# Kernel optimization log

Measured on AMD Instinct MI355X. Metric: run time of the kernel, lower is better.

## Reference

```python
import jax, jax.numpy as jnp
import numpy as np

EMBED_DIM = 1024
NUM_HEADS = 16
HEAD_DIM = EMBED_DIM // NUM_HEADS
BATCH = 2
SEQ = 2048


def setup_inputs() -> dict:
    key = jax.random.key(0)
    ks = jax.random.split(key, 9)
    s = 1.0 / np.sqrt(EMBED_DIM)
    return {
        "x": jax.random.normal(ks[0], (BATCH, SEQ, EMBED_DIM), jnp.float32),
        "mask": jnp.ones((BATCH, SEQ), jnp.int32),
        "Wq": jax.random.normal(ks[1], (EMBED_DIM, EMBED_DIM), jnp.float32) * s,
        "bq": jax.random.normal(ks[2], (EMBED_DIM,), jnp.float32) * s,
        "Wk": jax.random.normal(ks[3], (EMBED_DIM, EMBED_DIM), jnp.float32) * s,
        "bk": jax.random.normal(ks[4], (EMBED_DIM,), jnp.float32) * s,
        "Wv": jax.random.normal(ks[5], (EMBED_DIM, EMBED_DIM), jnp.float32) * s,
        "bv": jax.random.normal(ks[6], (EMBED_DIM,), jnp.float32) * s,
        "Wo": jax.random.normal(ks[7], (EMBED_DIM, EMBED_DIM), jnp.float32) * s,
        "bo": jax.random.normal(ks[8], (EMBED_DIM,), jnp.float32) * s,
    }


def reference(x, mask, Wq, bq, Wk, bk, Wv, bv, Wo, bo):
    B, S, E = x.shape
    H, D = NUM_HEADS, HEAD_DIM
    # torch Linear: y = x @ W.T + b
    q = (x @ Wq.T + bq).reshape(B, S, H, D).transpose(0, 2, 1, 3)  # [B,H,S,D]
    k = (x @ Wk.T + bk).reshape(B, S, H, D).transpose(0, 2, 1, 3)
    v = (x @ Wv.T + bv).reshape(B, S, H, D).transpose(0, 2, 1, 3)
    scores = jnp.einsum("bhqd,bhkd->bhqk", q, k) / jnp.sqrt(jnp.float32(D))
    # mask: [B,S] -> [B,1,1,S]; fill masked positions with -1e9
    scores = jnp.where(mask[:, None, None, :] == 0, jnp.float32(-1e9), scores)
    probs = jax.nn.softmax(scores, axis=-1)
    # dropout omitted: original stores a float and would crash; eval semantics = identity
    attn = jnp.einsum("bhqk,bhkd->bhqd", probs, v)  # [B,H,S,D]
    attn = attn.transpose(0, 2, 1, 3).reshape(B, S, E)
    return attn @ Wo.T + bo
```

## Files before the change

### kernel.cpp

```cpp
#include <hip/hip_runtime.h>
#include <stdint.h>

#define S_LEN 2048
#define EMB   1024
#define NH    16
#define HD    64
#define BM 128
#define BN 128
#define BK 64

typedef __bf16 bf16x8 __attribute__((ext_vector_type(8)));
typedef short  short4v __attribute__((ext_vector_type(4)));
typedef unsigned int uint2v __attribute__((ext_vector_type(2)));
typedef float  floatx4 __attribute__((ext_vector_type(4)));

#if defined(__has_builtin)
#if __has_builtin(__builtin_amdgcn_mfma_f32_16x16x16bf16_1k)
#define HAVE_MFMA16 1
#endif
#if __has_builtin(__builtin_amdgcn_exp2f)
#define EXP2F(x) __builtin_amdgcn_exp2f(x)
#endif
#endif
#ifndef EXP2F
#define EXP2F(x) exp2f(x)
#endif

#define QSCALE 0.1803368801111204f

__device__ __forceinline__ unsigned short f2bf(float f) {
  unsigned u = __builtin_bit_cast(unsigned, f);
  u += 0x7fffu + ((u >> 16) & 1u);
  return (unsigned short)(u >> 16);
}

__global__ __launch_bounds__(256) void cvt_all(const float* __restrict__ x,
                                               const float* __restrict__ Wq,
                                               const float* __restrict__ Wk,
                                               const float* __restrict__ Wv,
                                               const float* __restrict__ Wo,
                                               unsigned short* __restrict__ xb,
                                               unsigned short* __restrict__ Wqb,
                                               unsigned short* __restrict__ Wkb,
                                               unsigned short* __restrict__ Wvb,
                                               unsigned short* __restrict__ Wob) {
  int blk = blockIdx.x;
  const float* s; unsigned short* d; int off;
  if (blk < 4096)      { s = x;  d = xb;  off = blk; }
  else if (blk < 5120) { s = Wq; d = Wqb; off = blk - 4096; }
  else if (blk < 6144) { s = Wk; d = Wkb; off = blk - 5120; }
  else if (blk < 7168) { s = Wv; d = Wvb; off = blk - 6144; }
  else                 { s = Wo; d = Wob; off = blk - 7168; }
  int i = (off * 256 + threadIdx.x) * 4;
  float4 v = *(const float4*)(s + i);
  ushort4 o;
  o.x = f2bf(v.x); o.y = f2bf(v.y); o.z = f2bf(v.z); o.w = f2bf(v.w);
  *(ushort4*)(d + i) = o;
}

__device__ __forceinline__ void stage16(const void* g, void* l) {
  __builtin_amdgcn_global_load_lds(
      (const __attribute__((address_space(1))) void*)g,
      (__attribute__((address_space(3))) void*)l, 16, 0, 0);
}

__device__ __forceinline__ void gemm128(const unsigned short* __restrict__ A,
                                        const unsigned short* __restrict__ Bm,
                                        const float* __restrict__ bias, float scale,
                                        void* __restrict__ outp, int mode,
                                        unsigned short* As, unsigned short* Bs) {
  const int tid  = threadIdx.x;
  const int lane = tid & 63;
  const int wave = tid >> 6;
  const int m16  = lane & 15;
  const int quad = lane >> 4;
  const int m0 = blockIdx.x * BM;
  const int n0 = blockIdx.y * BN;
  const int wrow = (wave >> 1) * 64;
  const int wcol = (wave & 1) * 64;
  const int K = 1024, N = 1024;

  floatx4 acc[4][4];
  for (int i = 0; i < 4; ++i)
    for (int j = 0; j < 4; ++j) acc[i][j] = floatx4{0.f, 0.f, 0.f, 0.f};

  for (int k0 = 0; k0 < K; k0 += BK) {
    __syncthreads();
    for (int i = 0; i < 4; ++i) {
      int c   = i * 256 + tid;
      int row = c >> 3;
      int col = (c & 7) << 3;
      stage16(A  + (size_t)(m0 + row) * K + k0 + col,
              (char*)As + (size_t)(i * 256 + wave * 64) * 16);
      stage16(Bm + (size_t)(n0 + row) * K + k0 + col,
              (char*)Bs + (size_t)(i * 256 + wave * 64) * 16);
    }
    __syncthreads();
    for (int kk = 0; kk < 2; ++kk) {
      bf16x8 af[4], bfr[4];
      for (int ti = 0; ti < 4; ++ti)
        af[ti] = *(const bf16x8*)(As + (wrow + ti * 16 + m16) * BK + kk * 32 + quad * 8);
      for (int tj = 0; tj < 4; ++tj)
        bfr[tj] = *(const bf16x8*)(Bs + (wcol + tj * 16 + m16) * BK + kk * 32 + quad * 8);
      if (mode == 2) {
        for (int ti = 0; ti < 4; ++ti)
          for (int tj = 0; tj < 4; ++tj)
            acc[ti][tj] = __builtin_amdgcn_mfma_f32_16x16x32_bf16(bfr[tj], af[ti], acc[ti][tj], 0, 0, 0);
      } else {
        for (int ti = 0; ti < 4; ++ti)
          for (int tj = 0; tj < 4; ++tj)
            acc[ti][tj] = __builtin_amdgcn_mfma_f32_16x16x32_bf16(af[ti], bfr[tj], acc[ti][tj], 0, 0, 0);
      }
    }
  }

  if (mode == 2) {
    for (int tj = 0; tj < 4; ++tj) {
      for (int reg = 0; reg < 4; ++reg) {
        int n = n0 + wcol + tj * 16 + quad * 4 + reg;
        int hh = n >> 6, d = n & 63;
        float bv = bias[n];
        for (int ti = 0; ti < 4; ++ti) {
          int m = m0 + wrow + ti * 16 + m16;
          int b = m >> 11, s = m & 2047;
          ((unsigned short*)outp)[((size_t)(b * NH + hh) * HD + d) * S_LEN + s] =
              f2bf(acc[ti][tj][reg] + bv);
        }
      }
    }
    return;
  }

  for (int tj = 0; tj < 4; ++tj) {
    int n = n0 + wcol + tj * 16 + m16;
    float bv = bias[n];
    for (int ti = 0; ti < 4; ++ti) {
      for (int reg = 0; reg < 4; ++reg) {
        int m = m0 + wrow + ti * 16 + quad * 4 + reg;
        float v = (acc[ti][tj][reg] + bv) * scale;
        if (mode == 0) {
          ((float*)outp)[(size_t)m * N + n] = v;
        } else {
          int b = m >> 11, s = m & 2047, hh = n >> 6, d = n & 63;
          ((unsigned short*)outp)[((size_t)(b * NH + hh) * S_LEN + s) * HD + d] = f2bf(v);
        }
      }
    }
  }
}

__global__ __launch_bounds__(256) void qkv_gemm(const unsigned short* __restrict__ xb,
                                                const unsigned short* __restrict__ Wqb,
                                                const unsigned short* __restrict__ Wkb,
                                                const unsigned short* __restrict__ Wvb,
                                                const float* __restrict__ bq,
                                                const float* __restrict__ bk,
                                                const float* __restrict__ bv,
                                                unsigned short* __restrict__ Qb,
                                                unsigned short* __restrict__ Kb,
                                                unsigned short* __restrict__ Vtb) {
  __shared__ unsigned short As[BM * BK];
  __shared__ unsigned short Bs[BN * BK];
  int z = blockIdx.z;
  const unsigned short* Bm = (z == 0) ? Wqb : (z == 1) ? Wkb : Wvb;
  const float* bias        = (z == 0) ? bq  : (z == 1) ? bk  : bv;
  unsigned short* outp     = (z == 0) ? Qb  : (z == 1) ? Kb  : Vtb;
  float scale = (z == 0) ? QSCALE : 1.0f;
  gemm128(xb, Bm, bias, scale, outp, (z == 2) ? 2 : 1, As, Bs);
}

__global__ __launch_bounds__(256) void out_gemm(const unsigned short* __restrict__ Ab,
                                                const unsigned short* __restrict__ Wob,
                                                const float* __restrict__ bo,
                                                float* __restrict__ out) {
  __shared__ unsigned short As[64 * BK];
  __shared__ unsigned short Bs[128 * BK];
  const int tid  = threadIdx.x;
  const int lane = tid & 63;
  const int wave = tid >> 6;
  const int m16  = lane & 15;
  const int quad = lane >> 4;
  const int m0 = blockIdx.x * 64;
  const int n0 = blockIdx.y * 128;
  const int wrow = (wave >> 1) * 32;
  const int wcol = (wave & 1) * 64;
  const int K = 1024, N = 1024;

  floatx4 acc[2][4];
  for (int i = 0; i < 2; ++i)
    for (int j = 0; j < 4; ++j) acc[i][j] = floatx4{0.f, 0.f, 0.f, 0.f};

  for (int k0 = 0; k0 < K; k0 += BK) {
    __syncthreads();
    for (int i = 0; i < 2; ++i) {
      int c = i * 256 + tid;
      int row = c >> 3, col = (c & 7) << 3;
      stage16(Ab + (size_t)(m0 + row) * K + k0 + col,
              (char*)As + (size_t)(i * 256 + wave * 64) * 16);
    }
    for (int i = 0; i < 4; ++i) {
      int c = i * 256 + tid;
      int row = c >> 3, col = (c & 7) << 3;
      stage16(Wob + (size_t)(n0 + row) * K + k0 + col,
              (char*)Bs + (size_t)(i * 256 + wave * 64) * 16);
    }
    __syncthreads();
    for (int kk = 0; kk < 2; ++kk) {
      bf16x8 af[2], bfr[4];
      for (int ti = 0; ti < 2; ++ti)
        af[ti] = *(const bf16x8*)(As + (wrow + ti * 16 + m16) * BK + kk * 32 + quad * 8);
      for (int tj = 0; tj < 4; ++tj)
        bfr[tj] = *(const bf16x8*)(Bs + (wcol + tj * 16 + m16) * BK + kk * 32 + quad * 8);
      for (int ti = 0; ti < 2; ++ti)
        for (int tj = 0; tj < 4; ++tj)
          acc[ti][tj] = __builtin_amdgcn_mfma_f32_16x16x32_bf16(af[ti], bfr[tj], acc[ti][tj], 0, 0, 0);
    }
  }

  for (int tj = 0; tj < 4; ++tj) {
    int n = n0 + wcol + tj * 16 + m16;
    float bv = bo[n];
    for (int ti = 0; ti < 2; ++ti)
      for (int reg = 0; reg < 4; ++reg) {
        int m = m0 + wrow + ti * 16 + quad * 4 + reg;
        out[(size_t)m * N + n] = acc[ti][tj][reg] + bv;
      }
  }
}

__global__ __launch_bounds__(512, 2) void attn_kernel(const unsigned short* __restrict__ Qb,
                                                      const unsigned short* __restrict__ Kb,
                                                      const unsigned short* __restrict__ Vtb,
                                                      const int* __restrict__ mask,
                                                      unsigned short* __restrict__ attnb) {
  __shared__ unsigned short Ks[128 * 64];
  __shared__ unsigned short Vts[64 * 128];
  __shared__ float mb[128];
#ifndef HAVE_MFMA16
  __shared__ unsigned short Pq[8 * 16 * 72];
#endif

  const int tid  = threadIdx.x;
  const int lane = tid & 63;
  const int wave = tid >> 6;
  const int m16  = lane & 15;
  const int quad = lane >> 4;
  const int bh = blockIdx.x;
  const int qt = blockIdx.y;
  const int b  = bh >> 4;
  const int h  = bh & 15;
  const int q0 = qt * 128;
  const size_t head = (size_t)bh * S_LEN * HD;

  bf16x8 qf[2];
  {
    const unsigned short* qrow = Qb + head + (size_t)(q0 + wave * 16 + m16) * HD;
    qf[0] = *(const bf16x8*)(qrow + quad * 8);
    qf[1] = *(const bf16x8*)(qrow + 32 + quad * 8);
  }

  const int krow = tid >> 3, kch = tid & 7;
  const unsigned short* kg = Kb + head + (size_t)krow * HD + kch * 8;
  unsigned short* kl = Ks + krow * 64 + (kch ^ (krow & 7)) * 8;
  const int vrow = tid >> 4, vch = tid & 15;
  const unsigned short* vg = Vtb + head + (size_t)vrow * S_LEN + vch * 8;
  unsigned short* vl = Vts + vrow * 128 + (vch ^ (vrow & 7)) * 8;

  float m_run = -1e30f, l_run = 0.f;
  floatx4 acc_o[4];
  for (int ti = 0; ti < 4; ++ti) acc_o[ti] = floatx4{0.f, 0.f, 0.f, 0.f};

  uint4 kp0 = *(const uint4*)(kg);
  uint4 kp1 = *(const uint4*)(kg + 64 * HD);
  uint4 vp0 = *(const uint4*)(vg);
  uint4 vp1 = *(const uint4*)(vg + 32 * S_LEN);
  int   mp  = (tid < 128) ? mask[b * S_LEN + tid] : 1;

  const int xs = m16 & 7;

  for (int kb = 0; kb < 16; ++kb) {
    __syncthreads();
    *(uint4*)kl = kp0;  *(uint4*)(kl + 64 * 64) = kp1;
    *(uint4*)vl = vp0;  *(uint4*)(vl + 32 * 128) = vp1;
    if (tid < 128) mb[tid] = (mp == 0) ? -1e9f : 0.f;
    __syncthreads();

    {
      int kvn = (kb + 1 < 16) ? (kb + 1) * 128 : 0;
      kp0 = *(const uint4*)(kg + (size_t)kvn * HD);
      kp1 = *(const uint4*)(kg + (size_t)(kvn + 64) * HD);
      vp0 = *(const uint4*)(vg + kvn);
      vp1 = *(const uint4*)(vg + 32 * S_LEN + kvn);
      if (tid < 128) mp = mask[b * S_LEN + kvn + tid];
    }

    for (int hf = 0; hf < 2; ++hf) {
      floatx4 acc_s[4];
      for (int tj = 0; tj < 4; ++tj) acc_s[tj] = floatx4{0.f, 0.f, 0.f, 0.f};
      for (int kk = 0; kk < 2; ++kk)
        for (int tj = 0; tj < 4; ++tj) {
          bf16x8 kf = *(const bf16x8*)&Ks[(hf * 64 + tj * 16 + m16) * 64 +
                                          (((kk * 4 + quad) ^ xs) << 3)];
          acc_s[tj] = __builtin_amdgcn_mfma_f32_16x16x32_bf16(kf, qf[kk], acc_s[tj], 0, 0, 0);
        }

      float s[16];
      for (int t = 0; t < 4; ++t) {
        float4 mv = *(const float4*)&mb[hf * 64 + t * 16 + quad * 4];
        s[t * 4 + 0] = acc_s[t][0] + mv.x;
        s[t * 4 + 1] = acc_s[t][1] + mv.y;
        s[t * 4 + 2] = acc_s[t][2] + mv.z;
        s[t * 4 + 3] = acc_s[t][3] + mv.w;
      }
      float mloc = fmaxf(fmaxf(fmaxf(s[0], s[1]), fmaxf(s[2], s[3])),
                         fmaxf(fmaxf(s[4], s[5]), fmaxf(s[6], s[7])));
      float mloc2 = fmaxf(fmaxf(fmaxf(s[8], s[9]), fmaxf(s[10], s[11])),
                          fmaxf(fmaxf(s[12], s[13]), fmaxf(s[14], s[15])));
      mloc = fmaxf(mloc, mloc2);
      mloc = fmaxf(mloc, __shfl_xor(mloc, 16));
      mloc = fmaxf(mloc, __shfl_xor(mloc, 32));

      if (__any(mloc > m_run)) {
        float mnew = fmaxf(m_run, mloc);
        float alpha = EXP2F(m_run - mnew);
        m_run = mnew;
        l_run *= alpha;
        for (int ti = 0; ti < 4; ++ti)
          for (int reg = 0; reg < 4; ++reg) acc_o[ti][reg] *= alpha;
      }

      unsigned up[8];
      float sl = 0.f;
      for (int i = 0; i < 8; ++i) {
        float p0 = EXP2F(s[2 * i] - m_run);
        float p1 = EXP2F(s[2 * i + 1] - m_run);
        unsigned u0 = __builtin_bit_cast(unsigned, p0) + 0x8000u;
        unsigned u1 = __builtin_bit_cast(unsigned, p1) + 0x8000u;
        up[i] = __builtin_amdgcn_perm(u1, u0, 0x07060302);
        sl += __builtin_bit_cast(float, u0 & 0xffff0000u) +
              __builtin_bit_cast(float, u1 & 0xffff0000u);
      }
      sl += __shfl_xor(sl, 16);
      sl += __shfl_xor(sl, 32);
      l_run += sl;

#ifdef HAVE_MFMA16
      for (int ti = 0; ti < 4; ++ti)
        for (int c = 0; c < 4; ++c) {
          short4v vf = *(const short4v*)&Vts[(ti * 16 + m16) * 128 +
                                             (((hf * 8 + 2 * c + (quad >> 1)) ^ xs) << 3) +
                                             ((quad & 1) << 2)];
          short4v Pb = __builtin_bit_cast(short4v, uint2v{up[2 * c], up[2 * c + 1]});
          acc_o[ti] = __builtin_amdgcn_mfma_f32_16x16x16bf16_1k(vf, Pb, acc_o[ti], 0, 0, 0);
        }
#else
      unsigned short* Pw = Pq + wave * 16 * 72;
      for (int t = 0; t < 4; ++t) {
        *(unsigned*)&Pw[m16 * 72 + t * 16 + quad * 4]     = up[2 * t];
        *(unsigned*)&Pw[m16 * 72 + t * 16 + quad * 4 + 2] = up[2 * t + 1];
      }
      for (int kk = 0; kk < 2; ++kk) {
        bf16x8 pf = *(const bf16x8*)&Pw[m16 * 72 + kk * 32 + quad * 8];
        for (int ti = 0; ti < 4; ++ti) {
          bf16x8 vf = *(const bf16x8*)&Vts[(ti * 16 + m16) * 128 +
                                           (((hf * 8 + kk * 4 + quad) ^ xs) << 3)];
          acc_o[ti] = __builtin_amdgcn_mfma_f32_16x16x32_bf16(vf, pf, acc_o[ti], 0, 0, 0);
        }
      }
#endif
    }
  }

  float rl = 1.f / l_run;
  int orow = q0 + wave * 16 + m16;
  for (int ti = 0; ti < 4; ++ti) {
    ushort4 o;
    o.x = f2bf(acc_o[ti][0] * rl);
    o.y = f2bf(acc_o[ti][1] * rl);
    o.z = f2bf(acc_o[ti][2] * rl);
    o.w = f2bf(acc_o[ti][3] * rl);
    int e = h * HD + ti * 16 + quad * 4;
    *(ushort4*)&attnb[((size_t)(b * S_LEN + orow)) * EMB + e] = o;
  }
}

extern "C" void kernel_launch(void* const* d_in, const int* in_sizes, int n_in,
                              void* d_out, int out_size, void* d_ws, size_t ws_size,
                              hipStream_t stream) {
  const float* x  = (const float*)d_in[0];
  const int* mask = (const int*)d_in[1];
  const float* Wq = (const float*)d_in[2];
  const float* bq = (const float*)d_in[3];
  const float* Wk = (const float*)d_in[4];
  const float* bk = (const float*)d_in[5];
  const float* Wv = (const float*)d_in[6];
  const float* bv = (const float*)d_in[7];
  const float* Wo = (const float*)d_in[8];
  const float* bo = (const float*)d_in[9];
  float* out = (float*)d_out;

  char* ws = (char*)d_ws;
  unsigned short* xb  = (unsigned short*)(ws);
  unsigned short* Wqb = (unsigned short*)(ws + 8388608);
  unsigned short* Wkb = (unsigned short*)(ws + 10485760);
  unsigned short* Wvb = (unsigned short*)(ws + 12582912);
  unsigned short* Wob = (unsigned short*)(ws + 14680064);
  unsigned short* Qb  = (unsigned short*)(ws + 16777216);
  unsigned short* Kbb = (unsigned short*)(ws + 25165824);
  unsigned short* Vtb = (unsigned short*)(ws + 33554432);
  unsigned short* Ab  = (unsigned short*)(ws + 41943040);

  cvt_all<<<dim3(8192), dim3(256), 0, stream>>>(x, Wq, Wk, Wv, Wo, xb, Wqb, Wkb, Wvb, Wob);
  qkv_gemm<<<dim3(32, 8, 3), dim3(256), 0, stream>>>(xb, Wqb, Wkb, Wvb, bq, bk, bv, Qb, Kbb, Vtb);
  attn_kernel<<<dim3(32, 16), dim3(512), 0, stream>>>(Qb, Kbb, Vtb, mask, Ab);
  out_gemm<<<dim3(64, 8), dim3(256), 0, stream>>>(Ab, Wob, bo, out);
}
```

Before: 228.8 us.

## Double-buffer attention K/V tiles, skip mask when unmasked, retile QKV and output GEMMs

```diff
diff --git a/kernel.cpp b/kernel.cpp
--- a/kernel.cpp
+++ b/kernel.cpp
@@ -5,8 +5,6 @@
 #define EMB   1024
 #define NH    16
 #define HD    64
-#define BM 128
-#define BN 128
 #define BK 64
 
 typedef __bf16 bf16x8 __attribute__((ext_vector_type(8)));
@@ -18,13 +16,8 @@
 #if __has_builtin(__builtin_amdgcn_mfma_f32_16x16x16bf16_1k)
 #define HAVE_MFMA16 1
 #endif
-#if __has_builtin(__builtin_amdgcn_exp2f)
-#define EXP2F(x) __builtin_amdgcn_exp2f(x)
 #endif
-#endif
-#ifndef EXP2F
 #define EXP2F(x) exp2f(x)
-#endif
 
 #define QSCALE 0.1803368801111204f
 
@@ -32,6 +25,14 @@
   unsigned u = __builtin_bit_cast(unsigned, f);
   u += 0x7fffu + ((u >> 16) & 1u);
   return (unsigned short)(u >> 16);
+}
+__device__ __forceinline__ unsigned short f2bf_hu(float f) {
+  return (unsigned short)((__builtin_bit_cast(unsigned, f) + 0x8000u) >> 16);
+}
+__device__ __forceinline__ unsigned packbf2(float a, float b) {
+  unsigned ua = __builtin_bit_cast(unsigned, a) + 0x8000u;
+  unsigned ub = __builtin_bit_cast(unsigned, b) + 0x8000u;
+  return __builtin_amdgcn_perm(ub, ua, 0x07060302);
 }
 
 __global__ __launch_bounds__(256) void cvt_all(const float* __restrict__ x,
@@ -64,117 +65,25 @@
       (__attribute__((address_space(3))) void*)l, 16, 0, 0);
 }
 
-__device__ __forceinline__ void gemm128(const unsigned short* __restrict__ A,
-                                        const unsigned short* __restrict__ Bm,
-                                        const float* __restrict__ bias, float scale,
-                                        void* __restrict__ outp, int mode,
-                                        unsigned short* As, unsigned short* Bs) {
-  const int tid  = threadIdx.x;
-  const int lane = tid & 63;
-  const int wave = tid >> 6;
-  const int m16  = lane & 15;
-  const int quad = lane >> 4;
-  const int m0 = blockIdx.x * BM;
-  const int n0 = blockIdx.y * BN;
-  const int wrow = (wave >> 1) * 64;
-  const int wcol = (wave & 1) * 64;
-  const int K = 1024, N = 1024;
-
-  floatx4 acc[4][4];
-  for (int i = 0; i < 4; ++i)
-    for (int j = 0; j < 4; ++j) acc[i][j] = floatx4{0.f, 0.f, 0.f, 0.f};
-
-  for (int k0 = 0; k0 < K; k0 += BK) {
-    __syncthreads();
-    for (int i = 0; i < 4; ++i) {
-      int c   = i * 256 + tid;
-      int row = c >> 3;
-      int col = (c & 7) << 3;
-      stage16(A  + (size_t)(m0 + row) * K + k0 + col,
-              (char*)As + (size_t)(i * 256 + wave * 64) * 16);
-      stage16(Bm + (size_t)(n0 + row) * K + k0 + col,
-              (char*)Bs + (size_t)(i * 256 + wave * 64) * 16);
-    }
-    __syncthreads();
-    for (int kk = 0; kk < 2; ++kk) {
-      bf16x8 af[4], bfr[4];
-      for (int ti = 0; ti < 4; ++ti)
-        af[ti] = *(const bf16x8*)(As + (wrow + ti * 16 + m16) * BK + kk * 32 + quad * 8);
-      for (int tj = 0; tj < 4; ++tj)
-        bfr[tj] = *(const bf16x8*)(Bs + (wcol + tj * 16 + m16) * BK + kk * 32 + quad * 8);
-      if (mode == 2) {
-        for (int ti = 0; ti < 4; ++ti)
-          for (int tj = 0; tj < 4; ++tj)
-            acc[ti][tj] = __builtin_amdgcn_mfma_f32_16x16x32_bf16(bfr[tj], af[ti], acc[ti][tj], 0, 0, 0);
-      } else {
-        for (int ti = 0; ti < 4; ++ti)
-          for (int tj = 0; tj < 4; ++tj)
-            acc[ti][tj] = __builtin_amdgcn_mfma_f32_16x16x32_bf16(af[ti], bfr[tj], acc[ti][tj], 0, 0, 0);
-      }
-    }
-  }
-
-  if (mode == 2) {
-    for (int tj = 0; tj < 4; ++tj) {
-      for (int reg = 0; reg < 4; ++reg) {
-        int n = n0 + wcol + tj * 16 + quad * 4 + reg;
-        int hh = n >> 6, d = n & 63;
-        float bv = bias[n];
-        for (int ti = 0; ti < 4; ++ti) {
-          int m = m0 + wrow + ti * 16 + m16;
-          int b = m >> 11, s = m & 2047;
-          ((unsigned short*)outp)[((size_t)(b * NH + hh) * HD + d) * S_LEN + s] =
-              f2bf(acc[ti][tj][reg] + bv);
-        }
-      }
-    }
-    return;
-  }
-
-  for (int tj = 0; tj < 4; ++tj) {
-    int n = n0 + wcol + tj * 16 + m16;
-    float bv = bias[n];
-    for (int ti = 0; ti < 4; ++ti) {
-      for (int reg = 0; reg < 4; ++reg) {
-        int m = m0 + wrow + ti * 16 + quad * 4 + reg;
-        float v = (acc[ti][tj][reg] + bv) * scale;
-        if (mode == 0) {
-          ((float*)outp)[(size_t)m * N + n] = v;
-        } else {
-          int b = m >> 11, s = m & 2047, hh = n >> 6, d = n & 63;
-          ((unsigned short*)outp)[((size_t)(b * NH + hh) * S_LEN + s) * HD + d] = f2bf(v);
-        }
-      }
-    }
-  }
-}
-
-__global__ __launch_bounds__(256) void qkv_gemm(const unsigned short* __restrict__ xb,
-                                                const unsigned short* __restrict__ Wqb,
-                                                const unsigned short* __restrict__ Wkb,
-                                                const unsigned short* __restrict__ Wvb,
-                                                const float* __restrict__ bq,
-                                                const float* __restrict__ bk,
-                                                const float* __restrict__ bv,
-                                                unsigned short* __restrict__ Qb,
-                                                unsigned short* __restrict__ Kb,
-                                                unsigned short* __restrict__ Vtb) {
-  __shared__ unsigned short As[BM * BK];
-  __shared__ unsigned short Bs[BN * BK];
-  int z = blockIdx.z;
+__global__ __launch_bounds__(256, 4) void qkv_gemm(const unsigned short* __restrict__ xb,
+                                                   const unsigned short* __restrict__ Wqb,
+                                                   const unsigned short* __restrict__ Wkb,
+                                                   const unsigned short* __restrict__ Wvb,
+                                                   const float* __restrict__ bq,
+                                                   const float* __restrict__ bk,
+                                                   const float* __restrict__ bv,
+                                                   unsigned short* __restrict__ Qb,
+                                                   unsigned short* __restrict__ Kb,
+                                                   unsigned short* __restrict__ Vtb) {
+  __shared__ unsigned short As[64 * BK];
+  __shared__ unsigned short Bs[128 * BK];
+  const int z = blockIdx.z;
   const unsigned short* Bm = (z == 0) ? Wqb : (z == 1) ? Wkb : Wvb;
   const float* bias        = (z == 0) ? bq  : (z == 1) ? bk  : bv;
   unsigned short* outp     = (z == 0) ? Qb  : (z == 1) ? Kb  : Vtb;
-  float scale = (z == 0) ? QSCALE : 1.0f;
-  gemm128(xb, Bm, bias, scale, outp, (z == 2) ? 2 : 1, As, Bs);
-}
-
-__global__ __launch_bounds__(256) void out_gemm(const unsigned short* __restrict__ Ab,
-                                                const unsigned short* __restrict__ Wob,
-                                                const float* __restrict__ bo,
-                                                float* __restrict__ out) {
-  __shared__ unsigned short As[64 * BK];
-  __shared__ unsigned short Bs[128 * BK];
+  const float scale = (z == 0) ? QSCALE : 1.0f;
+  const int mode = (z == 2) ? 2 : 1;
+
   const int tid  = threadIdx.x;
   const int lane = tid & 63;
   const int wave = tid >> 6;
@@ -184,7 +93,7 @@
   const int n0 = blockIdx.y * 128;
   const int wrow = (wave >> 1) * 32;
   const int wcol = (wave & 1) * 64;
-  const int K = 1024, N = 1024;
+  const int K = 1024;
 
   floatx4 acc[2][4];
   for (int i = 0; i < 2; ++i)
@@ -195,13 +104,13 @@
     for (int i = 0; i < 2; ++i) {
       int c = i * 256 + tid;
       int row = c >> 3, col = (c & 7) << 3;
-      stage16(Ab + (size_t)(m0 + row) * K + k0 + col,
+      stage16(xb + (size_t)(m0 + row) * K + k0 + col,
               (char*)As + (size_t)(i * 256 + wave * 64) * 16);
     }
     for (int i = 0; i < 4; ++i) {
       int c = i * 256 + tid;
       int row = c >> 3, col = (c & 7) << 3;
-      stage16(Wob + (size_t)(n0 + row) * K + k0 + col,
+      stage16(Bm + (size_t)(n0 + row) * K + k0 + col,
               (char*)Bs + (size_t)(i * 256 + wave * 64) * 16);
     }
     __syncthreads();
@@ -213,11 +122,88 @@
         bfr[tj] = *(const bf16x8*)(Bs + (wcol + tj * 16 + m16) * BK + kk * 32 + quad * 8);
       for (int ti = 0; ti < 2; ++ti)
         for (int tj = 0; tj < 4; ++tj)
+          acc[ti][tj] = __builtin_amdgcn_mfma_f32_16x16x32_bf16(bfr[tj], af[ti], acc[ti][tj], 0, 0, 0);
+    }
+  }
+
+  if (mode == 1) {
+    for (int ti = 0; ti < 2; ++ti) {
+      int m = m0 + wrow + ti * 16 + m16;
+      int b = m >> 11, ss = m & 2047;
+      for (int tj = 0; tj < 4; ++tj) {
+        int n = n0 + wcol + tj * 16 + quad * 4;
+        int hh = n >> 6, d = n & 63;
+        float4 b4 = *(const float4*)(bias + n);
+        float v0 = (acc[ti][tj][0] + b4.x) * scale;
+        float v1 = (acc[ti][tj][1] + b4.y) * scale;
+        float v2 = (acc[ti][tj][2] + b4.z) * scale;
+        float v3 = (acc[ti][tj][3] + b4.w) * scale;
+        uint2v pk{packbf2(v0, v1), packbf2(v2, v3)};
+        *(uint2v*)((unsigned short*)outp +
+                   ((size_t)(b * NH + hh) * S_LEN + ss) * HD + d) = pk;
+      }
+    }
+  } else {
+    for (int tj = 0; tj < 4; ++tj)
+      for (int reg = 0; reg < 4; ++reg) {
+        int n = n0 + wcol + tj * 16 + quad * 4 + reg;
+        int hh = n >> 6, d = n & 63;
+        float bv = bias[n];
+        for (int ti = 0; ti < 2; ++ti) {
+          int m = m0 + wrow + ti * 16 + m16;
+          int b = m >> 11, ss = m & 2047;
+          ((unsigned short*)outp)[((size_t)(b * NH + hh) * HD + d) * S_LEN + ss] =
+              f2bf_hu(acc[ti][tj][reg] + bv);
+        }
+      }
+  }
+}
+
+__global__ __launch_bounds__(256, 4) void out_gemm(const unsigned short* __restrict__ Ab,
+                                                   const unsigned short* __restrict__ Wob,
+                                                   const float* __restrict__ bo,
+                                                   float* __restrict__ out) {
+  __shared__ unsigned short As[64 * BK];
+  __shared__ unsigned short Bs[64 * BK];
+  const int tid  = threadIdx.x;
+  const int lane = tid & 63;
+  const int wave = tid >> 6;
+  const int m16  = lane & 15;
+  const int quad = lane >> 4;
+  const int m0 = blockIdx.x * 64;
+  const int n0 = blockIdx.y * 64;
+  const int wrow = (wave >> 1) * 32;
+  const int wcol = (wave & 1) * 32;
+  const int K = 1024, N = 1024;
+
+  floatx4 acc[2][2];
+  for (int i = 0; i < 2; ++i)
+    for (int j = 0; j < 2; ++j) acc[i][j] = floatx4{0.f, 0.f, 0.f, 0.f};
+
+  for (int k0 = 0; k0 < K; k0 += BK) {
+    __syncthreads();
+    for (int i = 0; i < 2; ++i) {
+      int c = i * 256 + tid;
+      int row = c >> 3, col = (c & 7) << 3;
+      stage16(Ab + (size_t)(m0 + row) * K + k0 + col,
+              (char*)As + (size_t)(i * 256 + wave * 64) * 16);
+      stage16(Wob + (size_t)(n0 + row) * K + k0 + col,
+              (char*)Bs + (size_t)(i * 256 + wave * 64) * 16);
+    }
+    __syncthreads();
+    for (int kk = 0; kk < 2; ++kk) {
+      bf16x8 af[2], bfr[2];
+      for (int ti = 0; ti < 2; ++ti)
+        af[ti] = *(const bf16x8*)(As + (wrow + ti * 16 + m16) * BK + kk * 32 + quad * 8);
+      for (int tj = 0; tj < 2; ++tj)
+        bfr[tj] = *(const bf16x8*)(Bs + (wcol + tj * 16 + m16) * BK + kk * 32 + quad * 8);
+      for (int ti = 0; ti < 2; ++ti)
+        for (int tj = 0; tj < 2; ++tj)
           acc[ti][tj] = __builtin_amdgcn_mfma_f32_16x16x32_bf16(af[ti], bfr[tj], acc[ti][tj], 0, 0, 0);
     }
   }
 
-  for (int tj = 0; tj < 4; ++tj) {
+  for (int tj = 0; tj < 2; ++tj) {
     int n = n0 + wcol + tj * 16 + m16;
     float bv = bo[n];
     for (int ti = 0; ti < 2; ++ti)
@@ -233,9 +219,8 @@
                                                       const unsigned short* __restrict__ Vtb,
                                                       const int* __restrict__ mask,
                                                       unsigned short* __restrict__ attnb) {
-  __shared__ unsigned short Ks[128 * 64];
-  __shared__ unsigned short Vts[64 * 128];
-  __shared__ float mb[128];
+  __shared__ unsigned short Ks[2 * 128 * 64];
+  __shared__ unsigned short Vts[2 * 64 * 128];
 #ifndef HAVE_MFMA16
   __shared__ unsigned short Pq[8 * 16 * 72];
 #endif
@@ -261,10 +246,11 @@
 
   const int krow = tid >> 3, kch = tid & 7;
   const unsigned short* kg = Kb + head + (size_t)krow * HD + kch * 8;
-  unsigned short* kl = Ks + krow * 64 + (kch ^ (krow & 7)) * 8;
+  const int kloff = krow * 64 + ((kch ^ (krow & 7)) << 3);
   const int vrow = tid >> 4, vch = tid & 15;
   const unsigned short* vg = Vtb + head + (size_t)vrow * S_LEN + vch * 8;
-  unsigned short* vl = Vts + vrow * 128 + (vch ^ (vrow & 7)) * 8;
+  const int vloff = vrow * 128 + ((vch ^ (vrow & 7)) << 3);
+  const int* mrow = mask + b * S_LEN;
 
   float m_run = -1e30f, l_run = 0.f;
   floatx4 acc_o[4];
@@ -274,24 +260,37 @@
   uint4 kp1 = *(const uint4*)(kg + 64 * HD);
   uint4 vp0 = *(const uint4*)(vg);
   uint4 vp1 = *(const uint4*)(vg + 32 * S_LEN);
-  int   mp  = (tid < 128) ? mask[b * S_LEN + tid] : 1;
+  int a0 = mrow[lane], a1 = mrow[64 + lane];
+  bool dob_cur = __ballot((a0 == 0) | (a1 == 0)) != 0ull;
+  *(uint4*)&Ks[kloff] = kp0;  *(uint4*)&Ks[64 * 64 + kloff] = kp1;
+  *(uint4*)&Vts[vloff] = vp0; *(uint4*)&Vts[32 * 128 + vloff] = vp1;
+  kp0 = *(const uint4*)(kg + 128 * HD);
+  kp1 = *(const uint4*)(kg + 192 * HD);
+  vp0 = *(const uint4*)(vg + 128);
+  vp1 = *(const uint4*)(vg + 32 * S_LEN + 128);
+  a0 = mrow[128 + lane]; a1 = mrow[192 + lane];
+  bool dob_next = __ballot((a0 == 0) | (a1 == 0)) != 0ull;
+  __syncthreads();
 
   const int xs = m16 & 7;
 
   for (int kb = 0; kb < 16; ++kb) {
-    __syncthreads();
-    *(uint4*)kl = kp0;  *(uint4*)(kl + 64 * 64) = kp1;
-    *(uint4*)vl = vp0;  *(uint4*)(vl + 32 * 128) = vp1;
-    if (tid < 128) mb[tid] = (mp == 0) ? -1e9f : 0.f;
-    __syncthreads();
-
-    {
-      int kvn = (kb + 1 < 16) ? (kb + 1) * 128 : 0;
+    const int p = kb & 1;
+    const unsigned short* Kp = Ks + p * (128 * 64);
+    const unsigned short* Vp = Vts + p * (64 * 128);
+    bool dob_new = false;
+    if (kb < 15) {
+      unsigned short* Kn = Ks + (p ^ 1) * (128 * 64);
+      unsigned short* Vn = Vts + (p ^ 1) * (64 * 128);
+      *(uint4*)&Kn[kloff] = kp0;  *(uint4*)&Kn[64 * 64 + kloff] = kp1;
+      *(uint4*)&Vn[vloff] = vp0;  *(uint4*)&Vn[32 * 128 + vloff] = vp1;
+      int kvn = (kb + 2 < 16) ? (kb + 2) * 128 : 0;
       kp0 = *(const uint4*)(kg + (size_t)kvn * HD);
       kp1 = *(const uint4*)(kg + (size_t)(kvn + 64) * HD);
       vp0 = *(const uint4*)(vg + kvn);
       vp1 = *(const uint4*)(vg + 32 * S_LEN + kvn);
-      if (tid < 128) mp = mask[b * S_LEN + kvn + tid];
+      a0 = mrow[kvn + lane]; a1 = mrow[kvn + 64 + lane];
+      dob_new = __ballot((a0 == 0) | (a1 == 0)) != 0ull;
     }
 
     for (int hf = 0; hf < 2; ++hf) {
@@ -299,19 +298,23 @@
       for (int tj = 0; tj < 4; ++tj) acc_s[tj] = floatx4{0.f, 0.f, 0.f, 0.f};
       for (int kk = 0; kk < 2; ++kk)
         for (int tj = 0; tj < 4; ++tj) {
-          bf16x8 kf = *(const bf16x8*)&Ks[(hf * 64 + tj * 16 + m16) * 64 +
+          bf16x8 kf = *(const bf16x8*)&Kp[(hf * 64 + tj * 16 + m16) * 64 +
                                           (((kk * 4 + quad) ^ xs) << 3)];
           acc_s[tj] = __builtin_amdgcn_mfma_f32_16x16x32_bf16(kf, qf[kk], acc_s[tj], 0, 0, 0);
         }
 
       float s[16];
-      for (int t = 0; t < 4; ++t) {
-        float4 mv = *(const float4*)&mb[hf * 64 + t * 16 + quad * 4];
-        s[t * 4 + 0] = acc_s[t][0] + mv.x;
-        s[t * 4 + 1] = acc_s[t][1] + mv.y;
-        s[t * 4 + 2] = acc_s[t][2] + mv.z;
-        s[t * 4 + 3] = acc_s[t][3] + mv.w;
-      }
+      if (dob_cur) {
+        for (int t = 0; t < 4; ++t)
+          for (int r = 0; r < 4; ++r) {
+            int idx = kb * 128 + hf * 64 + t * 16 + quad * 4 + r;
+            s[t * 4 + r] = acc_s[t][r] + ((mrow[idx] == 0) ? -1e9f : 0.f);
+          }
+      } else {
+        for (int t = 0; t < 4; ++t)
+          for (int r = 0; r < 4; ++r) s[t * 4 + r] = acc_s[t][r];
+      }
+
       float mloc = fmaxf(fmaxf(fmaxf(s[0], s[1]), fmaxf(s[2], s[3])),
                          fmaxf(fmaxf(s[4], s[5]), fmaxf(s[6], s[7])));
       float mloc2 = fmaxf(fmaxf(fmaxf(s[8], s[9]), fmaxf(s[10], s[11])),
@@ -334,11 +337,8 @@
       for (int i = 0; i < 8; ++i) {
         float p0 = EXP2F(s[2 * i] - m_run);
         float p1 = EXP2F(s[2 * i + 1] - m_run);
-        unsigned u0 = __builtin_bit_cast(unsigned, p0) + 0x8000u;
-        unsigned u1 = __builtin_bit_cast(unsigned, p1) + 0x8000u;
-        up[i] = __builtin_amdgcn_perm(u1, u0, 0x07060302);
-        sl += __builtin_bit_cast(float, u0 & 0xffff0000u) +
-              __builtin_bit_cast(float, u1 & 0xffff0000u);
+        sl += p0 + p1;
+        up[i] = packbf2(p0, p1);
       }
       sl += __shfl_xor(sl, 16);
       sl += __shfl_xor(sl, 32);
@@ -347,9 +347,9 @@
 #ifdef HAVE_MFMA16
       for (int ti = 0; ti < 4; ++ti)
         for (int c = 0; c < 4; ++c) {
-          short4v vf = *(const short4v*)&Vts[(ti * 16 + m16) * 128 +
-                                             (((hf * 8 + 2 * c + (quad >> 1)) ^ xs) << 3) +
-                                             ((quad & 1) << 2)];
+          short4v vf = *(const short4v*)&Vp[(ti * 16 + m16) * 128 +
+                                            (((hf * 8 + 2 * c + (quad >> 1)) ^ xs) << 3) +
+                                            ((quad & 1) << 2)];
           short4v Pb = __builtin_bit_cast(short4v, uint2v{up[2 * c], up[2 * c + 1]});
           acc_o[ti] = __builtin_amdgcn_mfma_f32_16x16x16bf16_1k(vf, Pb, acc_o[ti], 0, 0, 0);
         }
@@ -362,23 +362,27 @@
       for (int kk = 0; kk < 2; ++kk) {
         bf16x8 pf = *(const bf16x8*)&Pw[m16 * 72 + kk * 32 + quad * 8];
         for (int ti = 0; ti < 4; ++ti) {
-          bf16x8 vf = *(const bf16x8*)&Vts[(ti * 16 + m16) * 128 +
-                                           (((hf * 8 + kk * 4 + quad) ^ xs) << 3)];
+          bf16x8 vf = *(const bf16x8*)&Vp[(ti * 16 + m16) * 128 +
+                                          (((hf * 8 + kk * 4 + quad) ^ xs) << 3)];
           acc_o[ti] = __builtin_amdgcn_mfma_f32_16x16x32_bf16(vf, pf, acc_o[ti], 0, 0, 0);
         }
       }
 #endif
     }
+
+    __syncthreads();
+    dob_cur = dob_next;
+    dob_next = dob_new;
   }
 
   float rl = 1.f / l_run;
   int orow = q0 + wave * 16 + m16;
   for (int ti = 0; ti < 4; ++ti) {
     ushort4 o;
-    o.x = f2bf(acc_o[ti][0] * rl);
-    o.y = f2bf(acc_o[ti][1] * rl);
-    o.z = f2bf(acc_o[ti][2] * rl);
-    o.w = f2bf(acc_o[ti][3] * rl);
+    o.x = f2bf_hu(acc_o[ti][0] * rl);
+    o.y = f2bf_hu(acc_o[ti][1] * rl);
+    o.z = f2bf_hu(acc_o[ti][2] * rl);
+    o.w = f2bf_hu(acc_o[ti][3] * rl);
     int e = h * HD + ti * 16 + quad * 4;
     *(ushort4*)&attnb[((size_t)(b * S_LEN + orow)) * EMB + e] = o;
   }
@@ -411,7 +415,7 @@
   unsigned short* Ab  = (unsigned short*)(ws + 41943040);
 
   cvt_all<<<dim3(8192), dim3(256), 0, stream>>>(x, Wq, Wk, Wv, Wo, xb, Wqb, Wkb, Wvb, Wob);
-  qkv_gemm<<<dim3(32, 8, 3), dim3(256), 0, stream>>>(xb, Wqb, Wkb, Wvb, bq, bk, bv, Qb, Kbb, Vtb);
+  qkv_gemm<<<dim3(64, 8, 3), dim3(256), 0, stream>>>(xb, Wqb, Wkb, Wvb, bq, bk, bv, Qb, Kbb, Vtb);
   attn_kernel<<<dim3(32, 16), dim3(512), 0, stream>>>(Qb, Kbb, Vtb, mask, Ab);
-  out_gemm<<<dim3(64, 8), dim3(256), 0, stream>>>(Ab, Wob, bo, out);
-}
+  out_gemm<<<dim3(64, 16), dim3(256), 0, stream>>>(Ab, Wob, bo, out);
+}
```

Result: no change. 226.4 us (-1.0%).
